# Performance work log

Hardware: AMD Instinct MI355X
Metric: run time of the kernel (lower is better)

The kernel has to match this reference:

```python
import jax, jax.numpy as jnp
import numpy as np

D_MODEL = 16
D_FF = 32
BLOCK = 64
B = 16384
EPS = 1e-5


def setup_inputs() -> dict:
    key = jax.random.key(0)
    ks = jax.random.split(key, 8)
    s = 1.0 / np.sqrt(D_MODEL)
    return {
        "x": jax.random.normal(ks[0], (B, BLOCK, D_MODEL), dtype=jnp.float32),
        # attention projections, stored as [in, out] so y = x @ W
        "Wk": jax.random.uniform(ks[1], (D_MODEL, D_MODEL), jnp.float32, -s, s),
        "Wq": jax.random.uniform(ks[2], (D_MODEL, D_MODEL), jnp.float32, -s, s),
        "Wv": jax.random.uniform(ks[3], (D_MODEL, D_MODEL), jnp.float32, -s, s),
        "ln1_g": jnp.ones((D_MODEL,), jnp.float32),
        "ln1_b": jnp.zeros((D_MODEL,), jnp.float32),
        "ln2_g": jnp.ones((D_MODEL,), jnp.float32),
        "ln2_b": jnp.zeros((D_MODEL,), jnp.float32),
        "W1": jax.random.uniform(ks[4], (D_MODEL, D_FF), jnp.float32, -s, s),
        "b1": jax.random.uniform(ks[5], (D_FF,), jnp.float32, -s, s),
        "W2": jax.random.uniform(ks[6], (D_FF, D_MODEL), jnp.float32, -1/np.sqrt(D_FF), 1/np.sqrt(D_FF)),
        "b2": jax.random.uniform(ks[7], (D_MODEL,), jnp.float32, -1/np.sqrt(D_FF), 1/np.sqrt(D_FF)),
    }


def _layernorm(x, g, b):
    mu = jnp.mean(x, axis=-1, keepdims=True)
    var = jnp.mean(jnp.square(x - mu), axis=-1, keepdims=True)
    return (x - mu) * jax.lax.rsqrt(var + EPS) * g + b


def reference(x, Wk, Wq, Wv, ln1_g, ln1_b, ln2_g, ln2_b, W1, b1, W2, b2):
    B_, T, C = x.shape
    h = _layernorm(x, ln1_g, ln1_b)
    k = h @ Wk
    q = h @ Wq
    v = h @ Wv
    att = jnp.einsum("btc,bsc->bts", q, k) / jnp.sqrt(jnp.float32(C))
    causal = jnp.tril(jnp.ones((T, T), dtype=bool))
    att = jnp.where(causal, att, -jnp.inf)
    att = jax.nn.softmax(att, axis=-1)
    y = jnp.einsum("bts,bsc->btc", att, v)
    x = x + y
    h2 = _layernorm(x, ln2_g, ln2_b)
    ff = jax.nn.gelu(h2 @ W1 + b1, approximate=False) @ W2 + b2
    return x + ff
```

## Files before the change

### kernel.cpp

```cpp
#include <hip/hip_runtime.h>
#include <hip/hip_bf16.h>
#include <math.h>


typedef __attribute__((ext_vector_type(8))) short bf8;
typedef __attribute__((ext_vector_type(4))) float f4;

union FragU { uint4 u4; uint u[4]; bf8 b; };

__device__ __forceinline__ uint packbf(float lo, float hi) {
    union { __hip_bfloat162 h; uint u; } c;
    c.h = __float22bfloat162_rn(make_float2(lo, hi));
    return c.u;
}

__device__ __forceinline__ float gelu_f(float u) {
    float z  = fabsf(u) * 0.70710678118654752f;
    float tt = __builtin_amdgcn_rcpf(1.f + 0.3275911f * z);
    float poly = ((((1.061405429f * tt - 1.453152027f) * tt + 1.421413741f) * tt
                   - 0.284496736f) * tt + 0.254829592f) * tt;
    float erfz = 1.f - poly * __expf(-z * z);
    return 0.5f * u * (1.f + copysignf(erfz, u));
}

#define MFMA(a, b, c) __builtin_amdgcn_mfma_f32_16x16x32_bf16(a, b, c, 0, 0, 0)

#define OQ  0
#define OK  768
#define OV  1536
#define OP  0
#define OH2 0
#define OU  768
#define OF  0
#define ARENA 2304

__device__ __forceinline__ void loadWfrag(const float* __restrict__ W, int ld,
                                          int n, int kb, bool valid, float scale,
                                          bf8& hf) {
    FragU H;
    if (valid) {
        #pragma unroll
        for (int p = 0; p < 4; ++p)
            H.u[p] = packbf(W[(kb+2*p)*ld+n]*scale, W[(kb+2*p+1)*ld+n]*scale);
    } else {
        H.u4 = make_uint4(0u,0u,0u,0u);
    }
    hf = H.b;
}

__global__ __launch_bounds__(64, 4)
void tb_kernel(const float* __restrict__ x,
               const float* __restrict__ Wk, const float* __restrict__ Wq,
               const float* __restrict__ Wv,
               const float* __restrict__ ln1g, const float* __restrict__ ln1b,
               const float* __restrict__ ln2g, const float* __restrict__ ln2b,
               const float* __restrict__ W1, const float* __restrict__ b1,
               const float* __restrict__ W2, const float* __restrict__ b2,
               float* __restrict__ out)
{
    __shared__ __align__(16) uint lds[ARENA];
    const int lane = threadIdx.x;
    const int c15  = lane & 15;
    const int quad = lane >> 4;
    const int quad4 = quad << 2;
    const size_t base = (size_t)blockIdx.x * (64 * 16);
    const f4 z4 = {0.f, 0.f, 0.f, 0.f};
    const bool kv = (quad < 2);
    const int  kb = quad * 8;
    const bool wrE = ((c15 & 1) == 0);

    bf8 fWq, fWk, fWv;
    loadWfrag(Wq, 16, c15, kb, kv, 0.25f, fWq);
    loadWfrag(Wk, 16, c15, kb, kv, 1.0f,  fWk);
    loadWfrag(Wv, 16, c15, kb, kv, 1.0f,  fWv);

    bf8 ah[4];
    {
        float gg[8], bb[8];
        if (kv) {
            const float4* gp = (const float4*)(ln1g + kb);
            const float4* bp = (const float4*)(ln1b + kb);
            float4 g0 = gp[0], g1 = gp[1], b0 = bp[0], b1_ = bp[1];
            gg[0]=g0.x; gg[1]=g0.y; gg[2]=g0.z; gg[3]=g0.w;
            gg[4]=g1.x; gg[5]=g1.y; gg[6]=g1.z; gg[7]=g1.w;
            bb[0]=b0.x; bb[1]=b0.y; bb[2]=b0.z; bb[3]=b0.w;
            bb[4]=b1_.x; bb[5]=b1_.y; bb[6]=b1_.z; bb[7]=b1_.w;
        }
        #pragma unroll
        for (int mt = 0; mt < 4; ++mt) {
            FragU Ah;
            if (kv) {
                const float4* xp = (const float4*)(x + base + (size_t)(mt*16 + c15)*16 + kb);
                float4 v0 = xp[0], v1 = xp[1];
                float xv[8] = {v0.x,v0.y,v0.z,v0.w, v1.x,v1.y,v1.z,v1.w};
                float s = 0.f;
                #pragma unroll
                for (int j = 0; j < 8; ++j) s += xv[j];
                s  += __shfl_xor(s, 16);
                float mu = s * 0.0625f;
                float s2 = 0.f;
                #pragma unroll
                for (int j = 0; j < 8; ++j) { float d = xv[j] - mu; s2 += d*d; }
                s2 += __shfl_xor(s2, 16);
                float var  = s2 * 0.0625f;
                float rstd = rsqrtf(var + 1e-5f);
                float h[8];
                #pragma unroll
                for (int j = 0; j < 8; ++j) h[j] = (xv[j]-mu)*rstd*gg[j] + bb[j];
                #pragma unroll
                for (int p = 0; p < 4; ++p) Ah.u[p] = packbf(h[2*p], h[2*p+1]);
            } else {
                Ah.u4 = make_uint4(0u,0u,0u,0u);
            }
            ah[mt] = Ah.b;
        }
    }

    #pragma unroll
    for (int mt = 0; mt < 4; ++mt) {
        f4 qc = MFMA(ah[mt], fWq, z4);
        f4 kc = MFMA(ah[mt], fWk, z4);
        f4 vc = MFMA(ah[mt], fWv, z4);
        #pragma unroll
        for (int r = 0; r < 4; ++r) {
            const int tok = mt*16 + quad4 + r;
            float qo = __shfl_xor(qc[r], 1);
            float ko = __shfl_xor(kc[r], 1);
            if (wrE) {
                lds[OQ + tok*12 + (c15>>1)] = packbf(qc[r], qo);
                lds[OK + tok*12 + (c15>>1)] = packbf(kc[r], ko);
            }
        }
        *(uint2*)(lds + OV + c15*36 + mt*8 + quad*2) =
            make_uint2(packbf(vc[0], vc[1]), packbf(vc[2], vc[3]));
    }
    __syncthreads();

    bf8 qb[4];
    #pragma unroll
    for (int qt = 0; qt < 4; ++qt) {
        FragU H;
        if (kv) H.u4 = *(const uint4*)(lds + OQ + (qt*16 + c15)*12 + quad4);
        else    H.u4 = make_uint4(0u,0u,0u,0u);
        qb[qt] = H.b;
    }
    f4 st[4][4];
    #pragma unroll
    for (int kt = 0; kt < 4; ++kt) {
        FragU H;
        if (kv) H.u4 = *(const uint4*)(lds + OK + (kt*16 + c15)*12 + quad4);
        else    H.u4 = make_uint4(0u,0u,0u,0u);
        bf8 ka = H.b;
        #pragma unroll
        for (int qt = 3; qt >= 0; --qt)
            if (qt >= kt)
                st[kt][qt] = MFMA(ka, qb[qt], z4);
    }
    #pragma unroll
    for (int qt = 0; qt < 4; ++qt)
        #pragma unroll
        for (int r = 0; r < 4; ++r)
            st[qt][qt][r] = (quad4 + r <= c15) ? st[qt][qt][r] : -1e30f;

    float linv[4];
    #pragma unroll
    for (int qt = 0; qt < 4; ++qt) {
        float mx = st[0][qt][0];
        #pragma unroll
        for (int kt = 0; kt < 4; ++kt) {
            if (kt <= qt) {
                #pragma unroll
                for (int r = 0; r < 4; ++r) mx = fmaxf(mx, st[kt][qt][r]);
            }
        }
        mx = fmaxf(mx, __shfl_xor(mx, 16));
        mx = fmaxf(mx, __shfl_xor(mx, 32));
        float l = 0.f;
        #pragma unroll
        for (int kt = 0; kt < 4; ++kt) {
            if (kt <= qt) {
                #pragma unroll
                for (int r = 0; r < 4; ++r) {
                    float p = __expf(st[kt][qt][r] - mx);
                    st[kt][qt][r] = p;
                    l += p;
                }
            }
        }
        l += __shfl_xor(l, 16);
        l += __shfl_xor(l, 32);
        linv[qt] = 1.0f / l;
    }

    bf8 va[2];
    #pragma unroll
    for (int kc = 0; kc < 2; ++kc) {
        FragU H;
        H.u4 = *(const uint4*)(lds + OV + c15*36 + kc*16 + quad4);
        va[kc] = H.b;
    }
    __syncthreads();

    #pragma unroll
    for (int qt = 0; qt < 4; ++qt) {
        const int rowo = OP + (qt*16 + c15)*36 + quad*2;
        #pragma unroll
        for (int kt = 0; kt < 4; ++kt) {
            uint2 w;
            if (kt <= qt) {
                w.x = packbf(st[kt][qt][0], st[kt][qt][1]);
                w.y = packbf(st[kt][qt][2], st[kt][qt][3]);
            } else w = make_uint2(0u, 0u);
            *(uint2*)(lds + rowo + kt*8) = w;
        }
    }
    __syncthreads();

    f4 yt[4];
    #pragma unroll
    for (int qt = 0; qt < 4; ++qt) {
        f4 acc = z4;
        #pragma unroll
        for (int kc = 0; kc < 2; ++kc) {
            if (kc == 0 || qt >= 2) {
                FragU P_;
                P_.u4 = *(const uint4*)(lds + OP + (qt*16 + c15)*36 + kc*16 + quad4);
                acc = MFMA(va[kc], P_.b, acc);
            }
        }
        yt[qt] = acc;
    }

    float x2v[4][4];
    #pragma unroll
    for (int qt = 0; qt < 4; ++qt) {
        float4 xv = *(const float4*)(x + base + (size_t)(qt*16 + c15)*16 + quad4);
        const float li = linv[qt];
        x2v[qt][0] = xv.x + yt[qt][0]*li;
        x2v[qt][1] = xv.y + yt[qt][1]*li;
        x2v[qt][2] = xv.z + yt[qt][2]*li;
        x2v[qt][3] = xv.w + yt[qt][3]*li;
    }
    __syncthreads();

    {
        float4 g2  = *(const float4*)(ln2g + quad4);
        float4 b2v = *(const float4*)(ln2b + quad4);
        #pragma unroll
        for (int qt = 0; qt < 4; ++qt) {
            float s = x2v[qt][0]+x2v[qt][1]+x2v[qt][2]+x2v[qt][3];
            s += __shfl_xor(s, 16); s += __shfl_xor(s, 32);
            float mu = s * 0.0625f;
            float d0 = x2v[qt][0]-mu, d1 = x2v[qt][1]-mu,
                  d2 = x2v[qt][2]-mu, d3 = x2v[qt][3]-mu;
            float s2 = d0*d0 + d1*d1 + d2*d2 + d3*d3;
            s2 += __shfl_xor(s2, 16); s2 += __shfl_xor(s2, 32);
            float rstd = rsqrtf(s2 * 0.0625f + 1e-5f);
            float h0 = d0*rstd*g2.x + b2v.x;
            float h1 = d1*rstd*g2.y + b2v.y;
            float h2_ = d2*rstd*g2.z + b2v.z;
            float h3 = d3*rstd*g2.w + b2v.w;
            *(uint2*)(lds + OH2 + (qt*16 + c15)*12 + quad*2) =
                make_uint2(packbf(h0, h1), packbf(h2_, h3));
        }
    }
    __syncthreads();

    bf8 a2[4];
    #pragma unroll
    for (int i = 0; i < 4; ++i) {
        FragU H;
        if (kv) H.u4 = *(const uint4*)(lds + OH2 + (i*16 + c15)*12 + quad4);
        else    H.u4 = make_uint4(0u,0u,0u,0u);
        a2[i] = H.b;
    }

    bf8 fW1a, fW1b, fW2;
    loadWfrag(W1, 32, c15,      kb, kv,   1.0f, fW1a);
    loadWfrag(W1, 32, c15 + 16, kb, kv,   1.0f, fW1b);
    loadWfrag(W2, 16, c15,      kb, true, 1.0f, fW2);

    {
        float bu0 = b1[c15], bu1 = b1[16 + c15];
        f4 cb0 = {bu0, bu0, bu0, bu0};
        f4 cb1 = {bu1, bu1, bu1, bu1};
        #pragma unroll
        for (int mt = 0; mt < 4; ++mt) {
            f4 u0 = MFMA(a2[mt], fW1a, cb0);
            f4 u1 = MFMA(a2[mt], fW1b, cb1);
            #pragma unroll
            for (int r = 0; r < 4; ++r) {
                float g0 = gelu_f(u0[r]);
                float g1 = gelu_f(u1[r]);
                float go0 = __shfl_xor(g0, 1);
                float go1 = __shfl_xor(g1, 1);
                if (wrE) {
                    const int row = mt*16 + quad4 + r;
                    lds[OU + row*20 +     (c15 >> 1)] = packbf(g0, go0);
                    lds[OU + row*20 + 8 + (c15 >> 1)] = packbf(g1, go1);
                }
            }
        }
    }
    __syncthreads();

    f4 fo[4];
    {
        float bo = b2[c15];
        f4 cb = {bo, bo, bo, bo};
        #pragma unroll
        for (int mt = 0; mt < 4; ++mt) {
            FragU H;
            H.u4 = *(const uint4*)(lds + OU + (mt*16 + c15)*20 + quad4);
            fo[mt] = MFMA(H.b, fW2, cb);
        }
    }
    __syncthreads();
    #pragma unroll
    for (int mt = 0; mt < 4; ++mt)
        #pragma unroll
        for (int r = 0; r < 4; ++r)
            lds[OF + (mt*16 + quad4 + r)*20 + c15] = __float_as_uint(fo[mt][r]);
    __syncthreads();

    #pragma unroll
    for (int qt = 0; qt < 4; ++qt) {
        FragU F;
        F.u4 = *(const uint4*)(lds + OF + (qt*16 + c15)*20 + quad4);
        float4 o;
        o.x = x2v[qt][0] + __uint_as_float(F.u[0]);
        o.y = x2v[qt][1] + __uint_as_float(F.u[1]);
        o.z = x2v[qt][2] + __uint_as_float(F.u[2]);
        o.w = x2v[qt][3] + __uint_as_float(F.u[3]);
        *(float4*)(out + base + (size_t)(qt*16 + c15)*16 + quad4) = o;
    }
}

extern "C" void kernel_launch(void* const* d_in, const int* in_sizes, int n_in,
                              void* d_out, int out_size, void* d_ws, size_t ws_size,
                              hipStream_t stream) {
    const float* x     = (const float*)d_in[0];
    const float* Wk    = (const float*)d_in[1];
    const float* Wq    = (const float*)d_in[2];
    const float* Wv    = (const float*)d_in[3];
    const float* ln1_g = (const float*)d_in[4];
    const float* ln1_b = (const float*)d_in[5];
    const float* ln2_g = (const float*)d_in[6];
    const float* ln2_b = (const float*)d_in[7];
    const float* W1    = (const float*)d_in[8];
    const float* b1    = (const float*)d_in[9];
    const float* W2    = (const float*)d_in[10];
    const float* b2    = (const float*)d_in[11];
    float* out = (float*)d_out;

    const int n_blocks = in_sizes[0] / (64 * 16);
    tb_kernel<<<n_blocks, 64, 0, stream>>>(
        x, Wk, Wq, Wv, ln1_g, ln1_b, ln2_g, ln2_b, W1, b1, W2, b2, out);
}
```

Baseline: 185.5 us.

## Process four sequences per workgroup and use exp2 softmax with folded log2e

Each workgroup now loops over four consecutive 64-token sequences, loading the weight fragments and biases once and reusing them across iterations. This cuts per-block weight-load and launch overhead, at the cost of fewer workgroups and serialized work per wave with no overlap between iterations. Separately, log2(e) is folded into the Wq scale so softmax can use the hardware exp2 and rcp intrinsics instead of __expf and a true division.

Measured after the change: 202.1 us. 8.9% more time.

```diff
diff --git a/kernel.cpp b/kernel.cpp
--- a/kernel.cpp
+++ b/kernel.cpp
@@ -7,6 +7,8 @@
 typedef __attribute__((ext_vector_type(4))) float f4;
 
 union FragU { uint4 u4; uint u[4]; bf8 b; };
+
+#define ITERS 4
 
 __device__ __forceinline__ uint packbf(float lo, float hi) {
     union { __hip_bfloat162 h; uint u; } c;
@@ -56,283 +58,288 @@
                const float* __restrict__ ln2g, const float* __restrict__ ln2b,
                const float* __restrict__ W1, const float* __restrict__ b1,
                const float* __restrict__ W2, const float* __restrict__ b2,
-               float* __restrict__ out)
+               float* __restrict__ out, int nblk)
 {
     __shared__ __align__(16) uint lds[ARENA];
     const int lane = threadIdx.x;
     const int c15  = lane & 15;
     const int quad = lane >> 4;
     const int quad4 = quad << 2;
-    const size_t base = (size_t)blockIdx.x * (64 * 16);
     const f4 z4 = {0.f, 0.f, 0.f, 0.f};
     const bool kv = (quad < 2);
     const int  kb = quad * 8;
     const bool wrE = ((c15 & 1) == 0);
 
     bf8 fWq, fWk, fWv;
-    loadWfrag(Wq, 16, c15, kb, kv, 0.25f, fWq);
+    loadWfrag(Wq, 16, c15, kb, kv, 0.25f*1.44269504f, fWq);
     loadWfrag(Wk, 16, c15, kb, kv, 1.0f,  fWk);
     loadWfrag(Wv, 16, c15, kb, kv, 1.0f,  fWv);
-
-    bf8 ah[4];
-    {
-        float gg[8], bb[8];
-        if (kv) {
-            const float4* gp = (const float4*)(ln1g + kb);
-            const float4* bp = (const float4*)(ln1b + kb);
-            float4 g0 = gp[0], g1 = gp[1], b0 = bp[0], b1_ = bp[1];
-            gg[0]=g0.x; gg[1]=g0.y; gg[2]=g0.z; gg[3]=g0.w;
-            gg[4]=g1.x; gg[5]=g1.y; gg[6]=g1.z; gg[7]=g1.w;
-            bb[0]=b0.x; bb[1]=b0.y; bb[2]=b0.z; bb[3]=b0.w;
-            bb[4]=b1_.x; bb[5]=b1_.y; bb[6]=b1_.z; bb[7]=b1_.w;
-        }
+    bf8 fW1a, fW1b, fW2f;
+    loadWfrag(W1, 32, c15,      kb, kv,   1.0f, fW1a);
+    loadWfrag(W1, 32, c15 + 16, kb, kv,   1.0f, fW1b);
+    loadWfrag(W2, 16, c15,      kb, true, 1.0f, fW2f);
+    const float bu0 = b1[c15], bu1 = b1[16 + c15], bo = b2[c15];
+
+    #pragma unroll 1
+    for (int it = 0; it < ITERS; ++it) {
+        const int blk = blockIdx.x * ITERS + it;
+        if (blk >= nblk) break;
+        const size_t base = (size_t)blk * (64 * 16);
+
+        bf8 ah[4];
+        {
+            float gg[8], bb[8];
+            if (kv) {
+                const float4* gp = (const float4*)(ln1g + kb);
+                const float4* bp = (const float4*)(ln1b + kb);
+                float4 g0 = gp[0], g1 = gp[1], b0 = bp[0], b1_ = bp[1];
+                gg[0]=g0.x; gg[1]=g0.y; gg[2]=g0.z; gg[3]=g0.w;
+                gg[4]=g1.x; gg[5]=g1.y; gg[6]=g1.z; gg[7]=g1.w;
+                bb[0]=b0.x; bb[1]=b0.y; bb[2]=b0.z; bb[3]=b0.w;
+                bb[4]=b1_.x; bb[5]=b1_.y; bb[6]=b1_.z; bb[7]=b1_.w;
+            }
+            #pragma unroll
+            for (int mt = 0; mt < 4; ++mt) {
+                FragU Ah;
+                if (kv) {
+                    const float4* xp = (const float4*)(x + base + (size_t)(mt*16 + c15)*16 + kb);
+                    float4 v0 = xp[0], v1 = xp[1];
+                    float xv[8] = {v0.x,v0.y,v0.z,v0.w, v1.x,v1.y,v1.z,v1.w};
+                    float s = 0.f;
+                    #pragma unroll
+                    for (int j = 0; j < 8; ++j) s += xv[j];
+                    s  += __shfl_xor(s, 16);
+                    float mu = s * 0.0625f;
+                    float s2 = 0.f;
+                    #pragma unroll
+                    for (int j = 0; j < 8; ++j) { float d = xv[j] - mu; s2 += d*d; }
+                    s2 += __shfl_xor(s2, 16);
+                    float var  = s2 * 0.0625f;
+                    float rstd = rsqrtf(var + 1e-5f);
+                    float h[8];
+                    #pragma unroll
+                    for (int j = 0; j < 8; ++j) h[j] = (xv[j]-mu)*rstd*gg[j] + bb[j];
+                    #pragma unroll
+                    for (int p = 0; p < 4; ++p) Ah.u[p] = packbf(h[2*p], h[2*p+1]);
+                } else {
+                    Ah.u4 = make_uint4(0u,0u,0u,0u);
+                }
+                ah[mt] = Ah.b;
+            }
+        }
+
         #pragma unroll
         for (int mt = 0; mt < 4; ++mt) {
-            FragU Ah;
-            if (kv) {
-                const float4* xp = (const float4*)(x + base + (size_t)(mt*16 + c15)*16 + kb);
-                float4 v0 = xp[0], v1 = xp[1];
-                float xv[8] = {v0.x,v0.y,v0.z,v0.w, v1.x,v1.y,v1.z,v1.w};
-                float s = 0.f;
-                #pragma unroll
-                for (int j = 0; j < 8; ++j) s += xv[j];
-                s  += __shfl_xor(s, 16);
+            f4 qc = MFMA(ah[mt], fWq, z4);
+            f4 kc = MFMA(ah[mt], fWk, z4);
+            f4 vc = MFMA(ah[mt], fWv, z4);
+            #pragma unroll
+            for (int r = 0; r < 4; ++r) {
+                const int tok = mt*16 + quad4 + r;
+                float qo = __shfl_xor(qc[r], 1);
+                float ko = __shfl_xor(kc[r], 1);
+                if (wrE) {
+                    lds[OQ + tok*12 + (c15>>1)] = packbf(qc[r], qo);
+                    lds[OK + tok*12 + (c15>>1)] = packbf(kc[r], ko);
+                }
+            }
+            *(uint2*)(lds + OV + c15*36 + mt*8 + quad*2) =
+                make_uint2(packbf(vc[0], vc[1]), packbf(vc[2], vc[3]));
+        }
+        __syncthreads();
+
+        bf8 qb[4];
+        #pragma unroll
+        for (int qt = 0; qt < 4; ++qt) {
+            FragU H;
+            if (kv) H.u4 = *(const uint4*)(lds + OQ + (qt*16 + c15)*12 + quad4);
+            else    H.u4 = make_uint4(0u,0u,0u,0u);
+            qb[qt] = H.b;
+        }
+        f4 st[4][4];
+        #pragma unroll
+        for (int kt = 0; kt < 4; ++kt) {
+            FragU H;
+            if (kv) H.u4 = *(const uint4*)(lds + OK + (kt*16 + c15)*12 + quad4);
+            else    H.u4 = make_uint4(0u,0u,0u,0u);
+            bf8 ka = H.b;
+            #pragma unroll
+            for (int qt = 3; qt >= 0; --qt)
+                if (qt >= kt)
+                    st[kt][qt] = MFMA(ka, qb[qt], z4);
+        }
+        #pragma unroll
+        for (int qt = 0; qt < 4; ++qt)
+            #pragma unroll
+            for (int r = 0; r < 4; ++r)
+                st[qt][qt][r] = (quad4 + r <= c15) ? st[qt][qt][r] : -1e30f;
+
+        float linv[4];
+        #pragma unroll
+        for (int qt = 0; qt < 4; ++qt) {
+            float mx = st[0][qt][0];
+            #pragma unroll
+            for (int kt = 0; kt < 4; ++kt) {
+                if (kt <= qt) {
+                    #pragma unroll
+                    for (int r = 0; r < 4; ++r) mx = fmaxf(mx, st[kt][qt][r]);
+                }
+            }
+            mx = fmaxf(mx, __shfl_xor(mx, 16));
+            mx = fmaxf(mx, __shfl_xor(mx, 32));
+            float l = 0.f;
+            #pragma unroll
+            for (int kt = 0; kt < 4; ++kt) {
+                if (kt <= qt) {
+                    #pragma unroll
+                    for (int r = 0; r < 4; ++r) {
+                        float p = __builtin_amdgcn_exp2f(st[kt][qt][r] - mx);
+                        st[kt][qt][r] = p;
+                        l += p;
+                    }
+                }
+            }
+            l += __shfl_xor(l, 16);
+            l += __shfl_xor(l, 32);
+            linv[qt] = __builtin_amdgcn_rcpf(l);
+        }
+
+        bf8 va[2];
+        #pragma unroll
+        for (int kc = 0; kc < 2; ++kc) {
+            FragU H;
+            H.u4 = *(const uint4*)(lds + OV + c15*36 + kc*16 + quad4);
+            va[kc] = H.b;
+        }
+        __syncthreads();
+
+        #pragma unroll
+        for (int qt = 0; qt < 4; ++qt) {
+            const int rowo = OP + (qt*16 + c15)*36 + quad*2;
+            #pragma unroll
+            for (int kt = 0; kt < 4; ++kt) {
+                uint2 w;
+                if (kt <= qt) {
+                    w.x = packbf(st[kt][qt][0], st[kt][qt][1]);
+                    w.y = packbf(st[kt][qt][2], st[kt][qt][3]);
+                } else w = make_uint2(0u, 0u);
+                *(uint2*)(lds + rowo + kt*8) = w;
+            }
+        }
+        __syncthreads();
+
+        f4 yt[4];
+        #pragma unroll
+        for (int qt = 0; qt < 4; ++qt) {
+            f4 acc = z4;
+            #pragma unroll
+            for (int kc = 0; kc < 2; ++kc) {
+                if (kc == 0 || qt >= 2) {
+                    FragU P_;
+                    P_.u4 = *(const uint4*)(lds + OP + (qt*16 + c15)*36 + kc*16 + quad4);
+                    acc = MFMA(va[kc], P_.b, acc);
+                }
+            }
+            yt[qt] = acc;
+        }
+
+        float x2v[4][4];
+        #pragma unroll
+        for (int qt = 0; qt < 4; ++qt) {
+            float4 xv = *(const float4*)(x + base + (size_t)(qt*16 + c15)*16 + quad4);
+            const float li = linv[qt];
+            x2v[qt][0] = xv.x + yt[qt][0]*li;
+            x2v[qt][1] = xv.y + yt[qt][1]*li;
+            x2v[qt][2] = xv.z + yt[qt][2]*li;
+            x2v[qt][3] = xv.w + yt[qt][3]*li;
+        }
+        __syncthreads();
+
+        {
+            float4 g2  = *(const float4*)(ln2g + quad4);
+            float4 b2v = *(const float4*)(ln2b + quad4);
+            #pragma unroll
+            for (int qt = 0; qt < 4; ++qt) {
+                float s = x2v[qt][0]+x2v[qt][1]+x2v[qt][2]+x2v[qt][3];
+                s += __shfl_xor(s, 16); s += __shfl_xor(s, 32);
                 float mu = s * 0.0625f;
-                float s2 = 0.f;
-                #pragma unroll
-                for (int j = 0; j < 8; ++j) { float d = xv[j] - mu; s2 += d*d; }
-                s2 += __shfl_xor(s2, 16);
-                float var  = s2 * 0.0625f;
-                float rstd = rsqrtf(var + 1e-5f);
-                float h[8];
-                #pragma unroll
-                for (int j = 0; j < 8; ++j) h[j] = (xv[j]-mu)*rstd*gg[j] + bb[j];
-                #pragma unroll
-                for (int p = 0; p < 4; ++p) Ah.u[p] = packbf(h[2*p], h[2*p+1]);
-            } else {
-                Ah.u4 = make_uint4(0u,0u,0u,0u);
-            }
-            ah[mt] = Ah.b;
-        }
-    }
-
-    #pragma unroll
-    for (int mt = 0; mt < 4; ++mt) {
-        f4 qc = MFMA(ah[mt], fWq, z4);
-        f4 kc = MFMA(ah[mt], fWk, z4);
-        f4 vc = MFMA(ah[mt], fWv, z4);
-        #pragma unroll
-        for (int r = 0; r < 4; ++r) {
-            const int tok = mt*16 + quad4 + r;
-            float qo = __shfl_xor(qc[r], 1);
-            float ko = __shfl_xor(kc[r], 1);
-            if (wrE) {
-                lds[OQ + tok*12 + (c15>>1)] = packbf(qc[r], qo);
-                lds[OK + tok*12 + (c15>>1)] = packbf(kc[r], ko);
-            }
-        }
-        *(uint2*)(lds + OV + c15*36 + mt*8 + quad*2) =
-            make_uint2(packbf(vc[0], vc[1]), packbf(vc[2], vc[3]));
-    }
-    __syncthreads();
-
-    bf8 qb[4];
-    #pragma unroll
-    for (int qt = 0; qt < 4; ++qt) {
-        FragU H;
-        if (kv) H.u4 = *(const uint4*)(lds + OQ + (qt*16 + c15)*12 + quad4);
-        else    H.u4 = make_uint4(0u,0u,0u,0u);
-        qb[qt] = H.b;
-    }
-    f4 st[4][4];
-    #pragma unroll
-    for (int kt = 0; kt < 4; ++kt) {
-        FragU H;
-        if (kv) H.u4 = *(const uint4*)(lds + OK + (kt*16 + c15)*12 + quad4);
-        else    H.u4 = make_uint4(0u,0u,0u,0u);
-        bf8 ka = H.b;
-        #pragma unroll
-        for (int qt = 3; qt >= 0; --qt)
-            if (qt >= kt)
-                st[kt][qt] = MFMA(ka, qb[qt], z4);
-    }
-    #pragma unroll
-    for (int qt = 0; qt < 4; ++qt)
-        #pragma unroll
-        for (int r = 0; r < 4; ++r)
-            st[qt][qt][r] = (quad4 + r <= c15) ? st[qt][qt][r] : -1e30f;
-
-    float linv[4];
-    #pragma unroll
-    for (int qt = 0; qt < 4; ++qt) {
-        float mx = st[0][qt][0];
-        #pragma unroll
-        for (int kt = 0; kt < 4; ++kt) {
-            if (kt <= qt) {
-                #pragma unroll
-                for (int r = 0; r < 4; ++r) mx = fmaxf(mx, st[kt][qt][r]);
-            }
-        }
-        mx = fmaxf(mx, __shfl_xor(mx, 16));
-        mx = fmaxf(mx, __shfl_xor(mx, 32));
-        float l = 0.f;
-        #pragma unroll
-        for (int kt = 0; kt < 4; ++kt) {
-            if (kt <= qt) {
+                float d0 = x2v[qt][0]-mu, d1 = x2v[qt][1]-mu,
+                      d2 = x2v[qt][2]-mu, d3 = x2v[qt][3]-mu;
+                float s2 = d0*d0 + d1*d1 + d2*d2 + d3*d3;
+                s2 += __shfl_xor(s2, 16); s2 += __shfl_xor(s2, 32);
+                float rstd = rsqrtf(s2 * 0.0625f + 1e-5f);
+                float h0 = d0*rstd*g2.x + b2v.x;
+                float h1 = d1*rstd*g2.y + b2v.y;
+                float h2_ = d2*rstd*g2.z + b2v.z;
+                float h3 = d3*rstd*g2.w + b2v.w;
+                *(uint2*)(lds + OH2 + (qt*16 + c15)*12 + quad*2) =
+                    make_uint2(packbf(h0, h1), packbf(h2_, h3));
+            }
+        }
+        __syncthreads();
+
+        bf8 a2[4];
+        #pragma unroll
+        for (int i = 0; i < 4; ++i) {
+            FragU H;
+            if (kv) H.u4 = *(const uint4*)(lds + OH2 + (i*16 + c15)*12 + quad4);
+            else    H.u4 = make_uint4(0u,0u,0u,0u);
+            a2[i] = H.b;
+        }
+
+        {
+            f4 cb0 = {bu0, bu0, bu0, bu0};
+            f4 cb1 = {bu1, bu1, bu1, bu1};
+            #pragma unroll
+            for (int mt = 0; mt < 4; ++mt) {
+                f4 u0 = MFMA(a2[mt], fW1a, cb0);
+                f4 u1 = MFMA(a2[mt], fW1b, cb1);
                 #pragma unroll
                 for (int r = 0; r < 4; ++r) {
-                    float p = __expf(st[kt][qt][r] - mx);
-                    st[kt][qt][r] = p;
-                    l += p;
-                }
-            }
-        }
-        l += __shfl_xor(l, 16);
-        l += __shfl_xor(l, 32);
-        linv[qt] = 1.0f / l;
-    }
-
-    bf8 va[2];
-    #pragma unroll
-    for (int kc = 0; kc < 2; ++kc) {
-        FragU H;
-        H.u4 = *(const uint4*)(lds + OV + c15*36 + kc*16 + quad4);
-        va[kc] = H.b;
-    }
-    __syncthreads();
-
-    #pragma unroll
-    for (int qt = 0; qt < 4; ++qt) {
-        const int rowo = OP + (qt*16 + c15)*36 + quad*2;
-        #pragma unroll
-        for (int kt = 0; kt < 4; ++kt) {
-            uint2 w;
-            if (kt <= qt) {
-                w.x = packbf(st[kt][qt][0], st[kt][qt][1]);
-                w.y = packbf(st[kt][qt][2], st[kt][qt][3]);
-            } else w = make_uint2(0u, 0u);
-            *(uint2*)(lds + rowo + kt*8) = w;
-        }
-    }
-    __syncthreads();
-
-    f4 yt[4];
-    #pragma unroll
-    for (int qt = 0; qt < 4; ++qt) {
-        f4 acc = z4;
-        #pragma unroll
-        for (int kc = 0; kc < 2; ++kc) {
-            if (kc == 0 || qt >= 2) {
-                FragU P_;
-                P_.u4 = *(const uint4*)(lds + OP + (qt*16 + c15)*36 + kc*16 + quad4);
-                acc = MFMA(va[kc], P_.b, acc);
-            }
-        }
-        yt[qt] = acc;
-    }
-
-    float x2v[4][4];
-    #pragma unroll
-    for (int qt = 0; qt < 4; ++qt) {
-        float4 xv = *(const float4*)(x + base + (size_t)(qt*16 + c15)*16 + quad4);
-        const float li = linv[qt];
-        x2v[qt][0] = xv.x + yt[qt][0]*li;
-        x2v[qt][1] = xv.y + yt[qt][1]*li;
-        x2v[qt][2] = xv.z + yt[qt][2]*li;
-        x2v[qt][3] = xv.w + yt[qt][3]*li;
-    }
-    __syncthreads();
-
-    {
-        float4 g2  = *(const float4*)(ln2g + quad4);
-        float4 b2v = *(const float4*)(ln2b + quad4);
-        #pragma unroll
-        for (int qt = 0; qt < 4; ++qt) {
-            float s = x2v[qt][0]+x2v[qt][1]+x2v[qt][2]+x2v[qt][3];
-            s += __shfl_xor(s, 16); s += __shfl_xor(s, 32);
-            float mu = s * 0.0625f;
-            float d0 = x2v[qt][0]-mu, d1 = x2v[qt][1]-mu,
-                  d2 = x2v[qt][2]-mu, d3 = x2v[qt][3]-mu;
-            float s2 = d0*d0 + d1*d1 + d2*d2 + d3*d3;
-            s2 += __shfl_xor(s2, 16); s2 += __shfl_xor(s2, 32);
-            float rstd = rsqrtf(s2 * 0.0625f + 1e-5f);
-            float h0 = d0*rstd*g2.x + b2v.x;
-            float h1 = d1*rstd*g2.y + b2v.y;
-            float h2_ = d2*rstd*g2.z + b2v.z;
-            float h3 = d3*rstd*g2.w + b2v.w;
-            *(uint2*)(lds + OH2 + (qt*16 + c15)*12 + quad*2) =
-                make_uint2(packbf(h0, h1), packbf(h2_, h3));
-        }
-    }
-    __syncthreads();
-
-    bf8 a2[4];
-    #pragma unroll
-    for (int i = 0; i < 4; ++i) {
-        FragU H;
-        if (kv) H.u4 = *(const uint4*)(lds + OH2 + (i*16 + c15)*12 + quad4);
-        else    H.u4 = make_uint4(0u,0u,0u,0u);
-        a2[i] = H.b;
-    }
-
-    bf8 fW1a, fW1b, fW2;
-    loadWfrag(W1, 32, c15,      kb, kv,   1.0f, fW1a);
-    loadWfrag(W1, 32, c15 + 16, kb, kv,   1.0f, fW1b);
-    loadWfrag(W2, 16, c15,      kb, true, 1.0f, fW2);
-
-    {
-        float bu0 = b1[c15], bu1 = b1[16 + c15];
-        f4 cb0 = {bu0, bu0, bu0, bu0};
-        f4 cb1 = {bu1, bu1, bu1, bu1};
-        #pragma unroll
-        for (int mt = 0; mt < 4; ++mt) {
-            f4 u0 = MFMA(a2[mt], fW1a, cb0);
-            f4 u1 = MFMA(a2[mt], fW1b, cb1);
-            #pragma unroll
-            for (int r = 0; r < 4; ++r) {
-                float g0 = gelu_f(u0[r]);
-                float g1 = gelu_f(u1[r]);
-                float go0 = __shfl_xor(g0, 1);
-                float go1 = __shfl_xor(g1, 1);
-                if (wrE) {
-                    const int row = mt*16 + quad4 + r;
-                    lds[OU + row*20 +     (c15 >> 1)] = packbf(g0, go0);
-                    lds[OU + row*20 + 8 + (c15 >> 1)] = packbf(g1, go1);
-                }
-            }
-        }
-    }
-    __syncthreads();
-
-    f4 fo[4];
-    {
-        float bo = b2[c15];
-        f4 cb = {bo, bo, bo, bo};
-        #pragma unroll
-        for (int mt = 0; mt < 4; ++mt) {
-            FragU H;
-            H.u4 = *(const uint4*)(lds + OU + (mt*16 + c15)*20 + quad4);
-            fo[mt] = MFMA(H.b, fW2, cb);
-        }
-    }
-    __syncthreads();
-    #pragma unroll
-    for (int mt = 0; mt < 4; ++mt)
-        #pragma unroll
-        for (int r = 0; r < 4; ++r)
-            lds[OF + (mt*16 + quad4 + r)*20 + c15] = __float_as_uint(fo[mt][r]);
-    __syncthreads();
-
-    #pragma unroll
-    for (int qt = 0; qt < 4; ++qt) {
-        FragU F;
-        F.u4 = *(const uint4*)(lds + OF + (qt*16 + c15)*20 + quad4);
-        float4 o;
-        o.x = x2v[qt][0] + __uint_as_float(F.u[0]);
-        o.y = x2v[qt][1] + __uint_as_float(F.u[1]);
-        o.z = x2v[qt][2] + __uint_as_float(F.u[2]);
-        o.w = x2v[qt][3] + __uint_as_float(F.u[3]);
-        *(float4*)(out + base + (size_t)(qt*16 + c15)*16 + quad4) = o;
+                    float g0 = gelu_f(u0[r]);
+                    float g1 = gelu_f(u1[r]);
+                    float go0 = __shfl_xor(g0, 1);
+                    float go1 = __shfl_xor(g1, 1);
+                    if (wrE) {
+                        const int row = mt*16 + quad4 + r;
+                        lds[OU + row*20 +     (c15 >> 1)] = packbf(g0, go0);
+                        lds[OU + row*20 + 8 + (c15 >> 1)] = packbf(g1, go1);
+                    }
+                }
+            }
+        }
+        __syncthreads();
+
+        f4 fo[4];
+        {
+            f4 cb = {bo, bo, bo, bo};
+            #pragma unroll
+            for (int mt = 0; mt < 4; ++mt) {
+                FragU H;
+                H.u4 = *(const uint4*)(lds + OU + (mt*16 + c15)*20 + quad4);
+                fo[mt] = MFMA(H.b, fW2f, cb);
+            }
+        }
+        __syncthreads();
+        #pragma unroll
+        for (int mt = 0; mt < 4; ++mt)
+            #pragma unroll
+            for (int r = 0; r < 4; ++r)
+                lds[OF + (mt*16 + quad4 + r)*20 + c15] = __float_as_uint(fo[mt][r]);
+        __syncthreads();
+
+        #pragma unroll
+        for (int qt = 0; qt < 4; ++qt) {
+            FragU F;
+            F.u4 = *(const uint4*)(lds + OF + (qt*16 + c15)*20 + quad4);
+            float4 o;
+            o.x = x2v[qt][0] + __uint_as_float(F.u[0]);
+            o.y = x2v[qt][1] + __uint_as_float(F.u[1]);
+            o.z = x2v[qt][2] + __uint_as_float(F.u[2]);
+            o.w = x2v[qt][3] + __uint_as_float(F.u[3]);
+            *(float4*)(out + base + (size_t)(qt*16 + c15)*16 + quad4) = o;
+        }
+        __syncthreads();
     }
 }
 
@@ -354,6 +361,7 @@
     float* out = (float*)d_out;
 
     const int n_blocks = in_sizes[0] / (64 * 16);
-    tb_kernel<<<n_blocks, 64, 0, stream>>>(
-        x, Wk, Wq, Wv, ln1_g, ln1_b, ln2_g, ln2_b, W1, b1, W2, b2, out);
-}
+    const int nwg = (n_blocks + ITERS - 1) / ITERS;
+    tb_kernel<<<nwg, 64, 0, stream>>>(
+        x, Wk, Wq, Wv, ln1_g, ln1_b, ln2_g, ln2_b, W1, b1, W2, b2, out, n_blocks);
+}
```

## Precompute weight fragments in a prep kernel and use cheaper softmax and GELU math

Applied to the files above, without the earlier changes.

Adds a one-block prep kernel that converts and packs all weight fragments, layernorm params and biases into a per-lane workspace, so each main block loads 13 uint4 values instead of gathering and converting fp32 weights itself. Softmax folds log2e into the Q scale and uses exp2 and a hardware reciprocal. The erf-based GELU is replaced by a sigmoid-style tanh approximation, which changes numerics slightly. It adds an extra kernel launch per call.

Result: faster. 173.4 us (-6.5%).

```diff
diff --git a/kernel.cpp b/kernel.cpp
--- a/kernel.cpp
+++ b/kernel.cpp
@@ -1,12 +1,12 @@
 #include <hip/hip_runtime.h>
 #include <hip/hip_bf16.h>
-#include <math.h>
 
 
 typedef __attribute__((ext_vector_type(8))) short bf8;
 typedef __attribute__((ext_vector_type(4))) float f4;
 
 union FragU { uint4 u4; uint u[4]; bf8 b; };
+union F4U  { uint4 u4; float4 f; };
 
 __device__ __forceinline__ uint packbf(float lo, float hi) {
     union { __hip_bfloat162 h; uint u; } c;
@@ -14,13 +14,11 @@
     return c.u;
 }
 
-__device__ __forceinline__ float gelu_f(float u) {
-    float z  = fabsf(u) * 0.70710678118654752f;
-    float tt = __builtin_amdgcn_rcpf(1.f + 0.3275911f * z);
-    float poly = ((((1.061405429f * tt - 1.453152027f) * tt + 1.421413741f) * tt
-                   - 0.284496736f) * tt + 0.254829592f) * tt;
-    float erfz = 1.f - poly * __expf(-z * z);
-    return 0.5f * u * (1.f + copysignf(erfz, u));
+__device__ __forceinline__ float gelu_fast(float u) {
+    float u2 = u * u;
+    float t  = u * (-2.3022079f + -0.1029431f * u2);
+    float e  = __builtin_amdgcn_exp2f(t);
+    return u * __builtin_amdgcn_rcpf(1.f + e);
 }
 
 #define MFMA(a, b, c) __builtin_amdgcn_mfma_f32_16x16x32_bf16(a, b, c, 0, 0, 0)
@@ -34,6 +32,8 @@
 #define OF  0
 #define ARENA 2304
 
+#define WS_SLOTS 16
+
 __device__ __forceinline__ void loadWfrag(const float* __restrict__ W, int ld,
                                           int n, int kb, bool valid, float scale,
                                           bf8& hf) {
@@ -48,14 +48,48 @@
     hf = H.b;
 }
 
+__global__ __launch_bounds__(64, 1)
+void prep_kernel(const float* __restrict__ Wk, const float* __restrict__ Wq,
+                 const float* __restrict__ Wv,
+                 const float* __restrict__ ln1g, const float* __restrict__ ln1b,
+                 const float* __restrict__ ln2g, const float* __restrict__ ln2b,
+                 const float* __restrict__ W1, const float* __restrict__ b1,
+                 const float* __restrict__ W2, const float* __restrict__ b2,
+                 uint4* __restrict__ ws)
+{
+    const int lane = threadIdx.x;
+    const int c15  = lane & 15;
+    const int quad = lane >> 4;
+    const int quad4 = quad << 2;
+    const bool kv = (quad < 2);
+    const int  kb = quad * 8;
+    uint4* o = ws + lane * WS_SLOTS;
+    FragU t; bf8 f;
+    loadWfrag(Wq, 16, c15, kb, kv, 0.25f*1.44269504f, f); t.b = f; o[0] = t.u4;
+    loadWfrag(Wk, 16, c15, kb, kv, 1.0f, f);              t.b = f; o[1] = t.u4;
+    loadWfrag(Wv, 16, c15, kb, kv, 1.0f, f);              t.b = f; o[2] = t.u4;
+    loadWfrag(W1, 32, c15,      kb, kv,   1.0f, f);       t.b = f; o[3] = t.u4;
+    loadWfrag(W1, 32, c15 + 16, kb, kv,   1.0f, f);       t.b = f; o[4] = t.u4;
+    loadWfrag(W2, 16, c15,      kb, true, 1.0f, f);       t.b = f; o[5] = t.u4;
+    F4U z; z.f = make_float4(0.f, 0.f, 0.f, 0.f);
+    F4U a, b;
+    if (kv) {
+        a.f = *(const float4*)(ln1g + kb); b.f = *(const float4*)(ln1g + kb + 4);
+    } else { a = z; b = z; }
+    o[6] = a.u4; o[7] = b.u4;
+    if (kv) {
+        a.f = *(const float4*)(ln1b + kb); b.f = *(const float4*)(ln1b + kb + 4);
+    } else { a = z; b = z; }
+    o[8] = a.u4; o[9] = b.u4;
+    a.f = *(const float4*)(ln2g + quad4); o[10] = a.u4;
+    a.f = *(const float4*)(ln2b + quad4); o[11] = a.u4;
+    a.f = make_float4(b1[c15], b1[c15 + 16], b2[c15], 0.f);
+    o[12] = a.u4;
+}
+
 __global__ __launch_bounds__(64, 4)
 void tb_kernel(const float* __restrict__ x,
-               const float* __restrict__ Wk, const float* __restrict__ Wq,
-               const float* __restrict__ Wv,
-               const float* __restrict__ ln1g, const float* __restrict__ ln1b,
-               const float* __restrict__ ln2g, const float* __restrict__ ln2b,
-               const float* __restrict__ W1, const float* __restrict__ b1,
-               const float* __restrict__ W2, const float* __restrict__ b2,
+               const uint4* __restrict__ ws,
                float* __restrict__ out)
 {
     __shared__ __align__(16) uint lds[ARENA];
@@ -69,23 +103,28 @@
     const int  kb = quad * 8;
     const bool wrE = ((c15 & 1) == 0);
 
-    bf8 fWq, fWk, fWv;
-    loadWfrag(Wq, 16, c15, kb, kv, 0.25f, fWq);
-    loadWfrag(Wk, 16, c15, kb, kv, 1.0f,  fWk);
-    loadWfrag(Wv, 16, c15, kb, kv, 1.0f,  fWv);
+    const uint4* wv = ws + lane * WS_SLOTS;
+    FragU t;
+    t.u4 = wv[0]; const bf8 fWq  = t.b;
+    t.u4 = wv[1]; const bf8 fWk  = t.b;
+    t.u4 = wv[2]; const bf8 fWv  = t.b;
+    t.u4 = wv[3]; const bf8 fW1a = t.b;
+    t.u4 = wv[4]; const bf8 fW1b = t.b;
+    t.u4 = wv[5]; const bf8 fW2f = t.b;
+    F4U fu;
+    fu.u4 = wv[6];  const float4 g1a = fu.f;
+    fu.u4 = wv[7];  const float4 g1b = fu.f;
+    fu.u4 = wv[8];  const float4 b1a = fu.f;
+    fu.u4 = wv[9];  const float4 b1b = fu.f;
+    fu.u4 = wv[10]; const float4 g2  = fu.f;
+    fu.u4 = wv[11]; const float4 b2v = fu.f;
+    fu.u4 = wv[12];
+    const float bu0 = fu.f.x, bu1 = fu.f.y, bo = fu.f.z;
 
     bf8 ah[4];
     {
-        float gg[8], bb[8];
-        if (kv) {
-            const float4* gp = (const float4*)(ln1g + kb);
-            const float4* bp = (const float4*)(ln1b + kb);
-            float4 g0 = gp[0], g1 = gp[1], b0 = bp[0], b1_ = bp[1];
-            gg[0]=g0.x; gg[1]=g0.y; gg[2]=g0.z; gg[3]=g0.w;
-            gg[4]=g1.x; gg[5]=g1.y; gg[6]=g1.z; gg[7]=g1.w;
-            bb[0]=b0.x; bb[1]=b0.y; bb[2]=b0.z; bb[3]=b0.w;
-            bb[4]=b1_.x; bb[5]=b1_.y; bb[6]=b1_.z; bb[7]=b1_.w;
-        }
+        const float gg[8] = {g1a.x,g1a.y,g1a.z,g1a.w, g1b.x,g1b.y,g1b.z,g1b.w};
+        const float bb[8] = {b1a.x,b1a.y,b1a.z,b1a.w, b1b.x,b1b.y,b1b.z,b1b.w};
         #pragma unroll
         for (int mt = 0; mt < 4; ++mt) {
             FragU Ah;
@@ -165,12 +204,14 @@
     float linv[4];
     #pragma unroll
     for (int qt = 0; qt < 4; ++qt) {
-        float mx = st[0][qt][0];
-        #pragma unroll
-        for (int kt = 0; kt < 4; ++kt) {
+        float mx = fmaxf(fmaxf(st[0][qt][0], st[0][qt][1]),
+                         fmaxf(st[0][qt][2], st[0][qt][3]));
+        #pragma unroll
+        for (int kt = 1; kt < 4; ++kt) {
             if (kt <= qt) {
-                #pragma unroll
-                for (int r = 0; r < 4; ++r) mx = fmaxf(mx, st[kt][qt][r]);
+                float mk = fmaxf(fmaxf(st[kt][qt][0], st[kt][qt][1]),
+                                 fmaxf(st[kt][qt][2], st[kt][qt][3]));
+                mx = fmaxf(mx, mk);
             }
         }
         mx = fmaxf(mx, __shfl_xor(mx, 16));
@@ -181,7 +222,7 @@
             if (kt <= qt) {
                 #pragma unroll
                 for (int r = 0; r < 4; ++r) {
-                    float p = __expf(st[kt][qt][r] - mx);
+                    float p = __builtin_amdgcn_exp2f(st[kt][qt][r] - mx);
                     st[kt][qt][r] = p;
                     l += p;
                 }
@@ -189,7 +230,7 @@
         }
         l += __shfl_xor(l, 16);
         l += __shfl_xor(l, 32);
-        linv[qt] = 1.0f / l;
+        linv[qt] = __builtin_amdgcn_rcpf(l);
     }
 
     bf8 va[2];
@@ -243,26 +284,22 @@
     }
     __syncthreads();
 
-    {
-        float4 g2  = *(const float4*)(ln2g + quad4);
-        float4 b2v = *(const float4*)(ln2b + quad4);
-        #pragma unroll
-        for (int qt = 0; qt < 4; ++qt) {
-            float s = x2v[qt][0]+x2v[qt][1]+x2v[qt][2]+x2v[qt][3];
-            s += __shfl_xor(s, 16); s += __shfl_xor(s, 32);
-            float mu = s * 0.0625f;
-            float d0 = x2v[qt][0]-mu, d1 = x2v[qt][1]-mu,
-                  d2 = x2v[qt][2]-mu, d3 = x2v[qt][3]-mu;
-            float s2 = d0*d0 + d1*d1 + d2*d2 + d3*d3;
-            s2 += __shfl_xor(s2, 16); s2 += __shfl_xor(s2, 32);
-            float rstd = rsqrtf(s2 * 0.0625f + 1e-5f);
-            float h0 = d0*rstd*g2.x + b2v.x;
-            float h1 = d1*rstd*g2.y + b2v.y;
-            float h2_ = d2*rstd*g2.z + b2v.z;
-            float h3 = d3*rstd*g2.w + b2v.w;
-            *(uint2*)(lds + OH2 + (qt*16 + c15)*12 + quad*2) =
-                make_uint2(packbf(h0, h1), packbf(h2_, h3));
-        }
+    #pragma unroll
+    for (int qt = 0; qt < 4; ++qt) {
+        float s = x2v[qt][0]+x2v[qt][1]+x2v[qt][2]+x2v[qt][3];
+        s += __shfl_xor(s, 16); s += __shfl_xor(s, 32);
+        float mu = s * 0.0625f;
+        float d0 = x2v[qt][0]-mu, d1 = x2v[qt][1]-mu,
+              d2 = x2v[qt][2]-mu, d3 = x2v[qt][3]-mu;
+        float s2 = d0*d0 + d1*d1 + d2*d2 + d3*d3;
+        s2 += __shfl_xor(s2, 16); s2 += __shfl_xor(s2, 32);
+        float rstd = rsqrtf(s2 * 0.0625f + 1e-5f);
+        float h0 = d0*rstd*g2.x + b2v.x;
+        float h1 = d1*rstd*g2.y + b2v.y;
+        float h2_ = d2*rstd*g2.z + b2v.z;
+        float h3 = d3*rstd*g2.w + b2v.w;
+        *(uint2*)(lds + OH2 + (qt*16 + c15)*12 + quad*2) =
+            make_uint2(packbf(h0, h1), packbf(h2_, h3));
     }
     __syncthreads();
 
@@ -275,13 +312,7 @@
         a2[i] = H.b;
     }
 
-    bf8 fW1a, fW1b, fW2;
-    loadWfrag(W1, 32, c15,      kb, kv,   1.0f, fW1a);
-    loadWfrag(W1, 32, c15 + 16, kb, kv,   1.0f, fW1b);
-    loadWfrag(W2, 16, c15,      kb, true, 1.0f, fW2);
-
     {
-        float bu0 = b1[c15], bu1 = b1[16 + c15];
         f4 cb0 = {bu0, bu0, bu0, bu0};
         f4 cb1 = {bu1, bu1, bu1, bu1};
         #pragma unroll
@@ -290,8 +321,8 @@
             f4 u1 = MFMA(a2[mt], fW1b, cb1);
             #pragma unroll
             for (int r = 0; r < 4; ++r) {
-                float g0 = gelu_f(u0[r]);
-                float g1 = gelu_f(u1[r]);
+                float g0 = gelu_fast(u0[r]);
+                float g1 = gelu_fast(u1[r]);
                 float go0 = __shfl_xor(g0, 1);
                 float go1 = __shfl_xor(g1, 1);
                 if (wrE) {
@@ -306,13 +337,12 @@
 
     f4 fo[4];
     {
-        float bo = b2[c15];
         f4 cb = {bo, bo, bo, bo};
         #pragma unroll
         for (int mt = 0; mt < 4; ++mt) {
             FragU H;
             H.u4 = *(const uint4*)(lds + OU + (mt*16 + c15)*20 + quad4);
-            fo[mt] = MFMA(H.b, fW2, cb);
+            fo[mt] = MFMA(H.b, fW2f, cb);
         }
     }
     __syncthreads();
@@ -352,8 +382,10 @@
     const float* W2    = (const float*)d_in[10];
     const float* b2    = (const float*)d_in[11];
     float* out = (float*)d_out;
-
+    uint4* ws = (uint4*)d_ws;
+
+    prep_kernel<<<1, 64, 0, stream>>>(Wk, Wq, Wv, ln1_g, ln1_b, ln2_g, ln2_b,
+                                      W1, b1, W2, b2, ws);
     const int n_blocks = in_sizes[0] / (64 * 16);
-    tb_kernel<<<n_blocks, 64, 0, stream>>>(
-        x, Wk, Wq, Wv, ln1_g, ln1_b, ln2_g, ln2_b, W1, b1, W2, b2, out);
-}
+    tb_kernel<<<n_blocks, 64, 0, stream>>>(x, ws, out);
+}
```
